# Performance work log

Measured on AMD Instinct MI355X. Metric: run time of the kernel, lower is better.

The kernel has to match this reference:

```python
import jax, jax.numpy as jnp
import numpy as np

B, CTX, DRAFT, D = 2, 4096, 512, 2048
H, KVH, HD = 16, 4, 128
N_REP = H // KVH
EPS = 1e-6
THETA = 10000.0
SCALE = 1.0 / np.sqrt(HD).astype(np.float32)


def setup_inputs() -> dict:
    key = jax.random.key(0)
    ks = jax.random.split(key, 6)
    return {
        "draft_hidden": jax.random.normal(ks[0], (B, DRAFT, D), jnp.float32),
        "context_hidden": jax.random.normal(ks[1], (B, CTX, D), jnp.float32),
        "Wq": jax.random.normal(ks[2], (H * HD, D), jnp.float32) * 0.02,
        "Wk": jax.random.normal(ks[3], (KVH * HD, D), jnp.float32) * 0.02,
        "Wv": jax.random.normal(ks[4], (KVH * HD, D), jnp.float32) * 0.02,
        "Wo": jax.random.normal(ks[5], (D, H * HD), jnp.float32) * 0.02,
        "q_norm_w": jnp.ones((HD,), jnp.float32),
        "k_norm_w": jnp.ones((HD,), jnp.float32),
        "context_position_ids": jnp.broadcast_to(jnp.arange(CTX, dtype=jnp.int32), (B, CTX)),
        "draft_position_ids": jnp.broadcast_to(CTX + jnp.arange(DRAFT, dtype=jnp.int32), (B, DRAFT)),
    }


def _rms_norm(x, w):
    # per-head RMSNorm over last dim (head_dim), computed in fp32
    v = jnp.mean(jnp.square(x.astype(jnp.float32)), axis=-1, keepdims=True)
    return (w * (x.astype(jnp.float32) * jax.lax.rsqrt(v + EPS))).astype(x.dtype)


def _rotate_half(x):
    x1, x2 = jnp.split(x, 2, axis=-1)
    return jnp.concatenate((-x2, x1), axis=-1)


def _rope(x, pos):
    # x: [B, nH, S, HD], pos: [B, S] int -> cos/sin gathered per position
    inv_freq = 1.0 / (THETA ** (jnp.arange(0, HD, 2, dtype=jnp.float32) / HD))  # [HD/2]
    freqs = pos.astype(jnp.float32)[:, None, :, None] * inv_freq  # [B,1,S,HD/2]
    emb = jnp.concatenate((freqs, freqs), axis=-1)  # [B,1,S,HD]
    return x * jnp.cos(emb) + _rotate_half(x) * jnp.sin(emb)


def reference(draft_hidden, context_hidden, Wq, Wk, Wv, Wo, q_norm_w, k_norm_w,
              context_position_ids, draft_position_ids):
    bsz, draft_len, _ = draft_hidden.shape
    ctx_len = context_hidden.shape[1]
    total_len = ctx_len + draft_len

    # Q from draft hidden only
    q = (draft_hidden @ Wq.T).reshape(bsz, draft_len, H, HD)
    q = _rms_norm(q, q_norm_w).transpose(0, 2, 1, 3)  # [B,H,Sq,HD]

    # Dual-source KV: context then draft, shared projections
    kv_in = jnp.concatenate([context_hidden, draft_hidden], axis=1)  # [B,total,D]
    k = (kv_in @ Wk.T).reshape(bsz, total_len, KVH, HD)
    v = (kv_in @ Wv.T).reshape(bsz, total_len, KVH, HD).transpose(0, 2, 1, 3)
    k = _rms_norm(k, k_norm_w).transpose(0, 2, 1, 3)  # [B,KVH,total,HD]

    full_position_ids = jnp.concatenate([context_position_ids, draft_position_ids], axis=1)
    q = _rope(q, draft_position_ids)
    k = _rope(k, full_position_ids)

    # GQA expansion (repeat each kv head n_rep times contiguously)
    k = jnp.repeat(k, N_REP, axis=1)  # [B,H,total,HD]
    v = jnp.repeat(v, N_REP, axis=1)

    # full (unmasked) scaled dot-product attention, block_mask=None path
    scores = jnp.einsum('bhqd,bhkd->bhqk', q, k) * SCALE
    probs = jax.nn.softmax(scores, axis=-1)
    attn = jnp.einsum('bhqk,bhkd->bhqd', probs, v)  # [B,H,Sq,HD]

    attn = attn.transpose(0, 2, 1, 3).reshape(bsz, draft_len, H * HD)
    return attn @ Wo.T
```

## Files before the change

### kernel.cpp

```cpp
#include <hip/hip_runtime.h>
#include <stdint.h>

#define B_ 2
#define CTX_ 4096
#define DRAFT_ 512
#define D_ 2048
#define H_ 16
#define KVH_ 4
#define HD_ 128
#define TOT_ 4608
#define NSPLIT 4
#define SPLIT_LEN (TOT_ / NSPLIT)

using bf16x8 = __attribute__((ext_vector_type(8))) short;
using f32x4  = __attribute__((ext_vector_type(4))) float;

__device__ __forceinline__ unsigned short f2bf(float x) {
  unsigned int u = __float_as_uint(x);
  u += 0x7fffu + ((u >> 16) & 1u);
  return (unsigned short)(u >> 16);
}

__device__ __forceinline__ unsigned cvtpk(float lo, float hi) {
  unsigned r;
  asm("v_cvt_pk_bf16_f32 %0, %1, %2" : "=v"(r) : "v"(lo), "v"(hi));
  return r;
}

__device__ __forceinline__ void gload16(const void* g, void* l) {
  __builtin_amdgcn_global_load_lds((const __attribute__((address_space(1))) void*)g,
                                   (__attribute__((address_space(3))) void*)l, 16, 0, 0);
}

__global__ __launch_bounds__(256, 4)
void conv_kernel(const float* __restrict__ ctx, const float* __restrict__ draft,
                 const float* __restrict__ wq, const float* __restrict__ wk,
                 const float* __restrict__ wv, const float* __restrict__ wo,
                 unsigned short* __restrict__ kv, unsigned short* __restrict__ wqb,
                 unsigned short* __restrict__ wkb, unsigned short* __restrict__ wvb,
                 unsigned short* __restrict__ wob) {
  long t = (long)blockIdx.x * 256 + threadIdx.x;
  const long NKV = (long)B_ * TOT_ * D_ / 8;
  const long NWQ = 2048L * 2048 / 8;
  const long NWK = 512L * 2048 / 8;
  const float* src;
  unsigned short* dst;
  if (t < NKV) {
    long i = t * 8;
    int b = (int)(i / ((long)TOT_ * D_));
    long rem = i - (long)b * TOT_ * D_;
    int r = (int)(rem / D_);
    int c = (int)(rem - (long)r * D_);
    if (r < CTX_) src = ctx + ((long)(b * CTX_ + r)) * D_ + c;
    else          src = draft + ((long)(b * DRAFT_ + (r - CTX_))) * D_ + c;
    dst = kv + i;
  } else if (t < NKV + NWQ) {
    long l = t - NKV; src = wq + l * 8; dst = wqb + l * 8;
  } else if (t < NKV + NWQ + NWK) {
    long l = t - NKV - NWQ; src = wk + l * 8; dst = wkb + l * 8;
  } else if (t < NKV + NWQ + 2 * NWK) {
    long l = t - NKV - NWQ - NWK; src = wv + l * 8; dst = wvb + l * 8;
  } else {
    long l = t - NKV - NWQ - 2 * NWK; src = wo + l * 8; dst = wob + l * 8;
  }
  float4 a = ((const float4*)src)[0];
  float4 b4 = ((const float4*)src)[1];
  uint4 o;
  o.x = (unsigned)f2bf(a.x) | ((unsigned)f2bf(a.y) << 16);
  o.y = (unsigned)f2bf(a.z) | ((unsigned)f2bf(a.w) << 16);
  o.z = (unsigned)f2bf(b4.x) | ((unsigned)f2bf(b4.y) << 16);
  o.w = (unsigned)f2bf(b4.z) | ((unsigned)f2bf(b4.w) << 16);
  *((uint4*)dst) = o;
}

template <int BM, int BN>
__device__ __forceinline__ void gemm_body(const unsigned short* __restrict__ A,
                                          const unsigned short* __restrict__ W,
                                          float* __restrict__ C, int ld, int kLen,
                                          int N, unsigned short* lds) {
  constexpr int MT = BM / 32;
  constexpr int NT = BN / 32;
  constexpr int BUF = (BM + BN) * 64;
  const int tid = threadIdx.x;
  const int lane = tid & 63, wid = tid >> 6;
  const int g = lane >> 4, r16 = lane & 15;
  const int wm = wid >> 1, wn = wid & 1;

  f32x4 zero = {0.f, 0.f, 0.f, 0.f};
  f32x4 acc[MT][NT];
#pragma unroll
  for (int i = 0; i < MT; ++i)
#pragma unroll
    for (int j = 0; j < NT; ++j) acc[i][j] = zero;

  auto stage = [&](int kb, unsigned short* buf) {
    unsigned short* As = buf;
    unsigned short* Bs = buf + BM * 64;
#pragma unroll
    for (int is = 0; is < BM / 32; ++is) {
      int row = is * 32 + (tid >> 3);
      int sl = (tid & 7) ^ (row & 7);
      gload16(A + (long)row * ld + kb + sl * 8, As + is * 2048 + wid * 512);
    }
#pragma unroll
    for (int is = 0; is < BN / 32; ++is) {
      int row = is * 32 + (tid >> 3);
      int sl = (tid & 7) ^ (row & 7);
      gload16(W + (long)row * ld + kb + sl * 8, Bs + is * 2048 + wid * 512);
    }
  };

  stage(0, lds);
  const int nk = kLen >> 6;
  for (int t = 0; t < nk; ++t) {
    __syncthreads();
    if (t + 1 < nk) stage((t + 1) << 6, lds + ((t + 1) & 1) * BUF);
    unsigned short* As = lds + (t & 1) * BUF;
    unsigned short* Bs = As + BM * 64;
#pragma unroll
    for (int kh = 0; kh < 2; ++kh) {
      bf16x8 af[MT], bfr[NT];
#pragma unroll
      for (int i = 0; i < MT; ++i) {
        int row = wm * (BM / 2) + i * 16 + r16;
        int sl = (kh * 4 + g) ^ (row & 7);
        af[i] = *(const bf16x8*)(As + row * 64 + sl * 8);
      }
#pragma unroll
      for (int j = 0; j < NT; ++j) {
        int row = wn * (BN / 2) + j * 16 + r16;
        int sl = (kh * 4 + g) ^ (row & 7);
        bfr[j] = *(const bf16x8*)(Bs + row * 64 + sl * 8);
      }
#pragma unroll
      for (int i = 0; i < MT; ++i)
#pragma unroll
        for (int j = 0; j < NT; ++j)
          acc[i][j] = __builtin_amdgcn_mfma_f32_16x16x32_bf16(af[i], bfr[j], acc[i][j], 0, 0, 0);
    }
  }
#pragma unroll
  for (int i = 0; i < MT; ++i)
#pragma unroll
    for (int j = 0; j < NT; ++j)
#pragma unroll
      for (int e = 0; e < 4; ++e) {
        int row = wm * (BM / 2) + i * 16 + g * 4 + e;
        int col = wn * (BN / 2) + j * 16 + r16;
        C[(long)row * N + col] = acc[i][j][e];
      }
}

__global__ __launch_bounds__(256, 2)
void qkv_kernel(const unsigned short* __restrict__ kvb,
                const unsigned short* __restrict__ wqb,
                const unsigned short* __restrict__ wkvb, float* __restrict__ qraw,
                float* __restrict__ kvraw) {
  __shared__ unsigned short lds[2 * 256 * 64];
  int id = blockIdx.x;
  if (id < 128) {
    int b = id >> 6, mb = (id >> 4) & 3, nb = id & 15;
    const unsigned short* A = kvb + ((long)b * TOT_ + CTX_ + mb * 128) * 2048;
    const unsigned short* W = wqb + (long)nb * 128 * 2048;
    float* C = qraw + ((long)b * 512 + mb * 128) * 2048 + nb * 128;
    gemm_body<128, 128>(A, W, C, 2048, 2048, 2048, lds);
  } else {
    int id2 = id - 128;
    int mb = id2 >> 3, nb = id2 & 7;
    const unsigned short* A = kvb + (long)mb * 128 * 2048;
    const unsigned short* W = wkvb + (long)nb * 128 * 2048;
    float* C = kvraw + (long)mb * 128 * 1024 + nb * 128;
    gemm_body<128, 128>(A, W, C, 2048, 2048, 1024, lds);
  }
}

__global__ __launch_bounds__(256, 3)
void ogemm_kernel(const unsigned short* __restrict__ attb,
                  const unsigned short* __restrict__ wob, float* __restrict__ oP) {
  __shared__ unsigned short lds[2 * 192 * 64];
  int mb = blockIdx.x, nb = blockIdx.y, z = blockIdx.z;
  const unsigned short* A = attb + (long)mb * 64 * 2048 + z * 1024;
  const unsigned short* W = wob + (long)nb * 128 * 2048 + z * 1024;
  float* C = oP + (long)z * 1024 * 2048 + (long)mb * 64 * 2048 + nb * 128;
  gemm_body<64, 128>(A, W, C, 2048, 1024, 2048, lds);
}

__global__ __launch_bounds__(256, 4)
void addo_kernel(const float* __restrict__ oP, float* __restrict__ out) {
  long t = (long)blockIdx.x * 256 + threadIdx.x;
  float4 a = ((const float4*)oP)[t];
  float4 b = ((const float4*)(oP + 1024L * 2048))[t];
  ((float4*)out)[t] = make_float4(a.x + b.x, a.y + b.y, a.z + b.z, a.w + b.w);
}

__global__ __launch_bounds__(256, 4)
void post_kernel(const float* __restrict__ qraw, const float* __restrict__ kvraw,
                 const float* __restrict__ qw, const float* __restrict__ kw,
                 const int* __restrict__ cpos, const int* __restrict__ dpos,
                 unsigned short* __restrict__ qatt, unsigned short* __restrict__ katt,
                 unsigned short* __restrict__ vt) {
  const int QB = (B_ * DRAFT_ * H_) / 4;
  const int KB = (B_ * TOT_ * KVH_) / 4;
  int bid = blockIdx.x;
  int tid = threadIdx.x;
  int lane = tid & 63, wid = tid >> 6;
  if (bid < QB + KB) {
    bool isQ = (bid < QB);
    int row = (isQ ? bid : bid - QB) * 4 + wid;
    const float* src;
    const float* wnorm;
    int pos;
    float fold;
    unsigned short* dst;
    if (isQ) {
      int b = row >> 13;
      int r2 = row & 8191;
      int s = r2 >> 4, hh = r2 & 15;
      src = qraw + (long)row * 128;
      wnorm = qw;
      pos = dpos[b * DRAFT_ + s];
      fold = 0.08838834764831843f * 1.4426950408889634f;
      dst = qatt + ((long)(b * H_ + hh) * DRAFT_ + s) * 128;
    } else {
      int b = row / (TOT_ * KVH_);
      int r2 = row - b * (TOT_ * KVH_);
      int s = r2 >> 2, hh = r2 & 3;
      src = kvraw + ((long)(b * TOT_ + s)) * 1024 + hh * 128;
      wnorm = kw;
      pos = (s < CTX_) ? cpos[b * CTX_ + s] : dpos[b * DRAFT_ + (s - CTX_)];
      fold = 1.0f;
      dst = katt + ((long)(b * KVH_ + hh) * TOT_ + s) * 128;
    }
    float x1 = src[lane], x2 = src[lane + 64];
    float ss = x1 * x1 + x2 * x2;
#pragma unroll
    for (int off = 1; off < 64; off <<= 1) ss += __shfl_xor(ss, off);
    float rn = rsqrtf(ss * 0.0078125f + 1e-6f);
    float y1 = wnorm[lane] * x1 * rn;
    float y2 = wnorm[lane + 64] * x2 * rn;
    float invf = exp2f((float)lane * -0.20762050593046014f);
    float fr = (float)pos * invf;
    float sn, cs;
    sincosf(fr, &sn, &cs);
    dst[lane] = f2bf((y1 * cs - y2 * sn) * fold);
    dst[lane + 64] = f2bf((y2 * cs + y1 * sn) * fold);
  } else {
    long t = (long)(bid - (QB + KB)) * 256 + tid;
    int d = (int)(t & 127);
    int rest = (int)(t >> 7);
    int sc = rest % 576, bk = rest / 576;
    int b = bk >> 2, kvh = bk & 3;
    int s0 = sc * 8;
    const float* src = kvraw + ((long)(b * TOT_ + s0)) * 1024 + 512 + kvh * 128 + d;
    unsigned int o[4];
#pragma unroll
    for (int jj = 0; jj < 4; ++jj) {
      unsigned short lo = f2bf(src[(2 * jj) * 1024]);
      unsigned short hi = f2bf(src[(2 * jj + 1) * 1024]);
      o[jj] = (unsigned)lo | ((unsigned)hi << 16);
    }
    uint4 ov = make_uint4(o[0], o[1], o[2], o[3]);
    *((uint4*)(vt + ((long)(bk * 128 + d)) * TOT_ + s0)) = ov;
  }
}

__global__ __launch_bounds__(256, 2)
void attn_kernel(const unsigned short* __restrict__ Q, const unsigned short* __restrict__ Kt,
                 const unsigned short* __restrict__ Vt, float* __restrict__ pO,
                 float* __restrict__ pL) {
  __shared__ unsigned short lds[2 * 16384 + 8192];
  unsigned short* P = lds + 32768;
  const int tid = threadIdx.x, lane = tid & 63, wid = tid >> 6;
  const int g = lane >> 4, r16 = lane & 15;
  const int q0 = blockIdx.x, h = blockIdx.y;
  const int b = blockIdx.z >> 2, split = blockIdx.z & 3;
  const int kvh = h >> 2;
  const float M = 16.4f;

  const unsigned short* Qbase =
      Q + ((long)(b * H_ + h) * DRAFT_ + q0 * 128 + wid * 32) * 128;
  bf16x8 qf[2][4];
#pragma unroll
  for (int f = 0; f < 2; ++f)
#pragma unroll
    for (int kb = 0; kb < 4; ++kb)
      qf[f][kb] = *(const bf16x8*)(Qbase + (f * 16 + r16) * 128 + kb * 32 + g * 8);

  f32x4 acc[2][8];
#pragma unroll
  for (int f = 0; f < 2; ++f)
#pragma unroll
    for (int nb = 0; nb < 8; ++nb) acc[f][nb] = f32x4{0.f, 0.f, 0.f, 0.f};
  float l_run[2] = {0.f, 0.f};

  const unsigned short* Kbase = Kt + (long)(b * KVH_ + kvh) * TOT_ * 128;
  const unsigned short* Vbase = Vt + (long)(b * KVH_ + kvh) * 128L * TOT_;

  auto stage = [&](int s0, int c) {
    unsigned short* Ks = lds + c * 16384;
    unsigned short* Vs = Ks + 8192;
#pragma unroll
    for (int is = 0; is < 4; ++is) {
      int row = is * 16 + (tid >> 4);
      int sl = (tid & 15) ^ (row & 7);
      gload16(Kbase + (long)(s0 + row) * 128 + sl * 8, Ks + is * 2048 + wid * 512);
    }
#pragma unroll
    for (int is = 0; is < 4; ++is) {
      int d = is * 32 + (tid >> 3);
      int sl = (tid & 7) ^ (d & 7);
      gload16(Vbase + (long)d * TOT_ + s0 + sl * 8, Vs + is * 2048 + wid * 512);
    }
  };

  const int sBeg = split * SPLIT_LEN;
  const int NTile = SPLIT_LEN / 64;
  stage(sBeg, 0);
  int cur = 0;
  for (int t = 0; t < NTile; ++t) {
    if (t + 1 < NTile) {
      stage(sBeg + (t + 1) * 64, cur ^ 1);
      asm volatile("s_waitcnt vmcnt(8)" ::: "memory");
    } else {
      asm volatile("s_waitcnt vmcnt(0)" ::: "memory");
    }
    __builtin_amdgcn_s_barrier();
    __builtin_amdgcn_sched_barrier(0);
    const unsigned short* Ks = lds + cur * 16384;
    const unsigned short* Vs = Ks + 8192;

    f32x4 st[2][4];
#pragma unroll
    for (int f = 0; f < 2; ++f)
#pragma unroll
      for (int h2 = 0; h2 < 4; ++h2) st[f][h2] = f32x4{-M, -M, -M, -M};
    __builtin_amdgcn_s_setprio(1);
#pragma unroll
    for (int h2 = 0; h2 < 4; ++h2) {
      int row = h2 * 16 + r16;
#pragma unroll
      for (int kb = 0; kb < 4; ++kb) {
        int sl = (kb * 4 + g) ^ (row & 7);
        bf16x8 a = *(const bf16x8*)(Ks + row * 128 + sl * 8);
        st[0][h2] = __builtin_amdgcn_mfma_f32_16x16x32_bf16(a, qf[0][kb], st[0][h2], 0, 0, 0);
        st[1][h2] = __builtin_amdgcn_mfma_f32_16x16x32_bf16(a, qf[1][kb], st[1][h2], 0, 0, 0);
      }
    }
    __builtin_amdgcn_s_setprio(0);

#pragma unroll
    for (int f = 0; f < 2; ++f) {
      float tsum = 0.0f;
#pragma unroll
      for (int h2 = 0; h2 < 4; ++h2)
#pragma unroll
        for (int e = 0; e < 4; ++e) {
          float p = exp2f(st[f][h2][e]);
          st[f][h2][e] = p;
          tsum += p;
        }
      tsum += __shfl_xor(tsum, 16);
      tsum += __shfl_xor(tsum, 32);
      l_run[f] += tsum;
      int qr = wid * 32 + f * 16 + r16;
#pragma unroll
      for (int h2 = 0; h2 < 4; ++h2) {
        unsigned lo = cvtpk(st[f][h2][0], st[f][h2][1]);
        unsigned hi = cvtpk(st[f][h2][2], st[f][h2][3]);
        int gr = (h2 * 2 + (g >> 1)) ^ (qr & 7);
        *(uint2*)((char*)P + qr * 128 + gr * 16 + (g & 1) * 8) = make_uint2(lo, hi);
      }
    }
    bf16x8 pb[2][2];
#pragma unroll
    for (int f = 0; f < 2; ++f) {
      int qr = wid * 32 + f * 16 + r16;
#pragma unroll
      for (int kb2 = 0; kb2 < 2; ++kb2) {
        int gr = (kb2 * 4 + g) ^ (qr & 7);
        pb[f][kb2] = *(const bf16x8*)((const char*)P + qr * 128 + gr * 16);
      }
    }
    __builtin_amdgcn_s_setprio(1);
#pragma unroll
    for (int nb = 0; nb < 8; ++nb) {
      int d = nb * 16 + r16;
#pragma unroll
      for (int kb2 = 0; kb2 < 2; ++kb2) {
        int sl = (kb2 * 4 + g) ^ (d & 7);
        bf16x8 a = *(const bf16x8*)(Vs + d * 64 + sl * 8);
        acc[0][nb] = __builtin_amdgcn_mfma_f32_16x16x32_bf16(a, pb[0][kb2], acc[0][nb], 0, 0, 0);
        acc[1][nb] = __builtin_amdgcn_mfma_f32_16x16x32_bf16(a, pb[1][kb2], acc[1][nb], 0, 0, 0);
      }
    }
    __builtin_amdgcn_s_setprio(0);
    __builtin_amdgcn_sched_barrier(0);
    __builtin_amdgcn_s_barrier();
    cur ^= 1;
  }

  const long R = (long)B_ * H_ * DRAFT_;
#pragma unroll
  for (int f = 0; f < 2; ++f) {
    int q = q0 * 128 + wid * 32 + f * 16 + r16;
    long rowIdx = ((long)(b * H_ + h)) * DRAFT_ + q;
    long pbase = ((long)split * R + rowIdx) * 128;
#pragma unroll
    for (int nb = 0; nb < 8; ++nb)
#pragma unroll
      for (int e = 0; e < 4; ++e) pO[pbase + nb * 16 + g * 4 + e] = acc[f][nb][e];
    if (g == 0) pL[(long)split * R + rowIdx] = l_run[f];
  }
}

__global__ __launch_bounds__(256, 4)
void acomb_kernel(const float* __restrict__ pO, const float* __restrict__ pL,
                  unsigned short* __restrict__ attb) {
  const long R = (long)B_ * H_ * DRAFT_;
  int row = blockIdx.x * 2 + (threadIdx.x >> 7);
  int d = threadIdx.x & 127;
  float ltot = 0.0f, o = 0.0f;
#pragma unroll
  for (int i = 0; i < NSPLIT; ++i) {
    ltot += pL[(long)i * R + row];
    o += pO[((long)i * R + row) * 128 + d];
  }
  o /= ltot;
  int bh = row >> 9, q = row & 511;
  int b = bh >> 4, h = bh & 15;
  attb[(((long)(b * 512 + q) * 16 + h)) * 128 + d] = f2bf(o);
}

extern "C" void kernel_launch(void* const* d_in, const int* in_sizes, int n_in,
                              void* d_out, int out_size, void* d_ws, size_t ws_size,
                              hipStream_t stream) {
  const float* draft = (const float*)d_in[0];
  const float* ctx = (const float*)d_in[1];
  const float* Wq = (const float*)d_in[2];
  const float* Wk = (const float*)d_in[3];
  const float* Wv = (const float*)d_in[4];
  const float* Wo = (const float*)d_in[5];
  const float* qw = (const float*)d_in[6];
  const float* kw = (const float*)d_in[7];
  const int* cpos = (const int*)d_in[8];
  const int* dpos = (const int*)d_in[9];

  char* ws = (char*)d_ws;
  unsigned short* kvb = (unsigned short*)(ws + 0);
  float* oP = (float*)(ws + 0);
  unsigned short* wqb = (unsigned short*)(ws + 37748736);
  unsigned short* wkb = (unsigned short*)(ws + 46137344);
  unsigned short* wvb = (unsigned short*)(ws + 48234496);
  unsigned short* wob = (unsigned short*)(ws + 50331648);
  float* qraw = (float*)(ws + 58720256);
  float* kvraw = (float*)(ws + 67108864);
  float* pO = (float*)(ws + 67108864);
  float* pL = (float*)(ws + 100663296);
  unsigned short* qatt = (unsigned short*)(ws + 104857600);
  unsigned short* katt = (unsigned short*)(ws + 109051904);
  unsigned short* vtb = (unsigned short*)(ws + 118489088);
  unsigned short* attb = (unsigned short*)(ws + 127926272);

  conv_kernel<<<dim3(14336), 256, 0, stream>>>(ctx, draft, Wq, Wk, Wv, Wo, kvb, wqb,
                                               wkb, wvb, wob);
  qkv_kernel<<<dim3(704), 256, 0, stream>>>(kvb, wqb, wkb, qraw, kvraw);
  post_kernel<<<dim3(15616), 256, 0, stream>>>(qraw, kvraw, qw, kw, cpos, dpos, qatt,
                                               katt, vtb);
  attn_kernel<<<dim3(4, 16, 2 * NSPLIT), 256, 0, stream>>>(qatt, katt, vtb, pO, pL);
  acomb_kernel<<<dim3(8192), 256, 0, stream>>>(pO, pL, attb);
  ogemm_kernel<<<dim3(16, 16, 2), 256, 0, stream>>>(attb, wob, oP);
  addo_kernel<<<dim3(2048), 256, 0, stream>>>(oP, (float*)d_out);
}
```

Measured before the change: 193.8 us.

## Switch attention to 32x32x16 MFMA with register-resident P and permuted V layout

Rewrites the attention inner loop to use 32x32x16 bf16 MFMAs, so the exponentiated score fragments can be repacked in registers as the B operand of the PV product. This drops the P round trip through LDS. The post kernel now writes V-transpose with a permuted k-order so it matches the 32x32 accumulator layout, and output stores become float4. Blocks of the attention and QKV GEMM grids are also remapped in an XCD-aware order to improve L2 locality. The main risks are register pressure from the larger accumulators and silent wrong results if the V permutation and the fragment mapping do not match exactly.

Result: faster. 180.9 us (-6.7%).

```diff
diff --git a/kernel.cpp b/kernel.cpp
--- a/kernel.cpp
+++ b/kernel.cpp
@@ -14,6 +14,7 @@
 
 using bf16x8 = __attribute__((ext_vector_type(8))) short;
 using f32x4  = __attribute__((ext_vector_type(4))) float;
+using f32x16 = __attribute__((ext_vector_type(16))) float;
 
 __device__ __forceinline__ unsigned short f2bf(float x) {
   unsigned int u = __float_as_uint(x);
@@ -30,6 +31,13 @@
 __device__ __forceinline__ void gload16(const void* g, void* l) {
   __builtin_amdgcn_global_load_lds((const __attribute__((address_space(1))) void*)g,
                                    (__attribute__((address_space(3))) void*)l, 16, 0, 0);
+}
+
+__device__ __forceinline__ f32x16 vbroad16(float x) {
+  f32x16 v;
+#pragma unroll
+  for (int i = 0; i < 16; ++i) v[i] = x;
+  return v;
 }
 
 __global__ __launch_bounds__(256, 4)
@@ -157,7 +165,7 @@
                 const unsigned short* __restrict__ wkvb, float* __restrict__ qraw,
                 float* __restrict__ kvraw) {
   __shared__ unsigned short lds[2 * 256 * 64];
-  int id = blockIdx.x;
+  int id = (blockIdx.x & 7) * 88 + (blockIdx.x >> 3);
   if (id < 128) {
     int b = id >> 6, mb = (id >> 4) & 3, nb = id & 15;
     const unsigned short* A = kvb + ((long)b * TOT_ + CTX_ + mb * 128) * 2048;
@@ -259,8 +267,10 @@
       unsigned short hi = f2bf(src[(2 * jj + 1) * 1024]);
       o[jj] = (unsigned)lo | ((unsigned)hi << 16);
     }
-    uint4 ov = make_uint4(o[0], o[1], o[2], o[3]);
-    *((uint4*)(vt + ((long)(bk * 128 + d)) * TOT_ + s0)) = ov;
+    int k0 = s0 & 63;
+    long dstbase = ((long)(bk * 128 + d)) * TOT_ + (s0 & ~63) + (k0 & 48) + ((k0 & 8) >> 1);
+    *(uint2*)(vt + dstbase) = make_uint2(o[0], o[1]);
+    *(uint2*)(vt + dstbase + 8) = make_uint2(o[2], o[3]);
   }
 }
 
@@ -268,30 +278,26 @@
 void attn_kernel(const unsigned short* __restrict__ Q, const unsigned short* __restrict__ Kt,
                  const unsigned short* __restrict__ Vt, float* __restrict__ pO,
                  float* __restrict__ pL) {
-  __shared__ unsigned short lds[2 * 16384 + 8192];
-  unsigned short* P = lds + 32768;
+  __shared__ unsigned short lds[2 * 16384];
   const int tid = threadIdx.x, lane = tid & 63, wid = tid >> 6;
-  const int g = lane >> 4, r16 = lane & 15;
-  const int q0 = blockIdx.x, h = blockIdx.y;
-  const int b = blockIdx.z >> 2, split = blockIdx.z & 3;
+  const int hi = lane >> 5, l31 = lane & 31;
+  int sw = ((blockIdx.x & 7) << 6) | (blockIdx.x >> 3);
+  const int q0 = sw & 3, h = (sw >> 2) & 15, z = sw >> 6;
+  const int b = z >> 2, split = z & 3;
   const int kvh = h >> 2;
   const float M = 16.4f;
 
-  const unsigned short* Qbase =
+  const unsigned short* Qb =
       Q + ((long)(b * H_ + h) * DRAFT_ + q0 * 128 + wid * 32) * 128;
-  bf16x8 qf[2][4];
-#pragma unroll
-  for (int f = 0; f < 2; ++f)
-#pragma unroll
-    for (int kb = 0; kb < 4; ++kb)
-      qf[f][kb] = *(const bf16x8*)(Qbase + (f * 16 + r16) * 128 + kb * 32 + g * 8);
-
-  f32x4 acc[2][8];
-#pragma unroll
-  for (int f = 0; f < 2; ++f)
-#pragma unroll
-    for (int nb = 0; nb < 8; ++nb) acc[f][nb] = f32x4{0.f, 0.f, 0.f, 0.f};
-  float l_run[2] = {0.f, 0.f};
+  bf16x8 qf[8];
+#pragma unroll
+  for (int ks = 0; ks < 8; ++ks)
+    qf[ks] = *(const bf16x8*)(Qb + l31 * 128 + ks * 16 + hi * 8);
+
+  f32x16 acc[4];
+#pragma unroll
+  for (int nb = 0; nb < 4; ++nb) acc[nb] = vbroad16(0.f);
+  float l_run = 0.0f;
 
   const unsigned short* Kbase = Kt + (long)(b * KVH_ + kvh) * TOT_ * 128;
   const unsigned short* Vbase = Vt + (long)(b * KVH_ + kvh) * 128L * TOT_;
@@ -326,71 +332,53 @@
     }
     __builtin_amdgcn_s_barrier();
     __builtin_amdgcn_sched_barrier(0);
-    const unsigned short* Ks = lds + cur * 16384;
-    const unsigned short* Vs = Ks + 8192;
-
-    f32x4 st[2][4];
-#pragma unroll
-    for (int f = 0; f < 2; ++f)
-#pragma unroll
-      for (int h2 = 0; h2 < 4; ++h2) st[f][h2] = f32x4{-M, -M, -M, -M};
+    const char* KsB = (const char*)(lds + cur * 16384);
+    const char* VsB = KsB + 16384;
+
+    f32x16 st0 = vbroad16(-M), st1 = vbroad16(-M);
     __builtin_amdgcn_s_setprio(1);
 #pragma unroll
-    for (int h2 = 0; h2 < 4; ++h2) {
-      int row = h2 * 16 + r16;
-#pragma unroll
-      for (int kb = 0; kb < 4; ++kb) {
-        int sl = (kb * 4 + g) ^ (row & 7);
-        bf16x8 a = *(const bf16x8*)(Ks + row * 128 + sl * 8);
-        st[0][h2] = __builtin_amdgcn_mfma_f32_16x16x32_bf16(a, qf[0][kb], st[0][h2], 0, 0, 0);
-        st[1][h2] = __builtin_amdgcn_mfma_f32_16x16x32_bf16(a, qf[1][kb], st[1][h2], 0, 0, 0);
-      }
+    for (int ks = 0; ks < 8; ++ks) {
+      int gsl = ks * 2 + hi;
+      bf16x8 a0 = *(const bf16x8*)(KsB + l31 * 256 + ((gsl ^ (l31 & 7)) * 16));
+      bf16x8 a1 = *(const bf16x8*)(KsB + (32 + l31) * 256 + ((gsl ^ (l31 & 7)) * 16));
+      st0 = __builtin_amdgcn_mfma_f32_32x32x16_bf16(a0, qf[ks], st0, 0, 0, 0);
+      st1 = __builtin_amdgcn_mfma_f32_32x32x16_bf16(a1, qf[ks], st1, 0, 0, 0);
     }
     __builtin_amdgcn_s_setprio(0);
 
-#pragma unroll
-    for (int f = 0; f < 2; ++f) {
-      float tsum = 0.0f;
-#pragma unroll
-      for (int h2 = 0; h2 < 4; ++h2)
-#pragma unroll
-        for (int e = 0; e < 4; ++e) {
-          float p = exp2f(st[f][h2][e]);
-          st[f][h2][e] = p;
-          tsum += p;
-        }
-      tsum += __shfl_xor(tsum, 16);
-      tsum += __shfl_xor(tsum, 32);
-      l_run[f] += tsum;
-      int qr = wid * 32 + f * 16 + r16;
-#pragma unroll
-      for (int h2 = 0; h2 < 4; ++h2) {
-        unsigned lo = cvtpk(st[f][h2][0], st[f][h2][1]);
-        unsigned hi = cvtpk(st[f][h2][2], st[f][h2][3]);
-        int gr = (h2 * 2 + (g >> 1)) ^ (qr & 7);
-        *(uint2*)((char*)P + qr * 128 + gr * 16 + (g & 1) * 8) = make_uint2(lo, hi);
-      }
-    }
-    bf16x8 pb[2][2];
-#pragma unroll
-    for (int f = 0; f < 2; ++f) {
-      int qr = wid * 32 + f * 16 + r16;
-#pragma unroll
-      for (int kb2 = 0; kb2 < 2; ++kb2) {
-        int gr = (kb2 * 4 + g) ^ (qr & 7);
-        pb[f][kb2] = *(const bf16x8*)((const char*)P + qr * 128 + gr * 16);
-      }
+    float l_own = 0.0f;
+    unsigned pkA[8], pkB[8];
+#pragma unroll
+    for (int m = 0; m < 8; ++m) {
+      float e0 = exp2f(st0[2 * m]), e1 = exp2f(st0[2 * m + 1]);
+      l_own += e0 + e1;
+      pkA[m] = cvtpk(e0, e1);
+    }
+#pragma unroll
+    for (int m = 0; m < 8; ++m) {
+      float e0 = exp2f(st1[2 * m]), e1 = exp2f(st1[2 * m + 1]);
+      l_own += e0 + e1;
+      pkB[m] = cvtpk(e0, e1);
+    }
+    l_run += l_own;
+
+    union { unsigned u[4]; bf16x8 v; } pf[4];
+#pragma unroll
+    for (int m = 0; m < 4; ++m) {
+      pf[0].u[m] = pkA[m];
+      pf[1].u[m] = pkA[m + 4];
+      pf[2].u[m] = pkB[m];
+      pf[3].u[m] = pkB[m + 4];
     }
     __builtin_amdgcn_s_setprio(1);
 #pragma unroll
-    for (int nb = 0; nb < 8; ++nb) {
-      int d = nb * 16 + r16;
-#pragma unroll
-      for (int kb2 = 0; kb2 < 2; ++kb2) {
-        int sl = (kb2 * 4 + g) ^ (d & 7);
-        bf16x8 a = *(const bf16x8*)(Vs + d * 64 + sl * 8);
-        acc[0][nb] = __builtin_amdgcn_mfma_f32_16x16x32_bf16(a, pb[0][kb2], acc[0][nb], 0, 0, 0);
-        acc[1][nb] = __builtin_amdgcn_mfma_f32_16x16x32_bf16(a, pb[1][kb2], acc[1][nb], 0, 0, 0);
+    for (int nb = 0; nb < 4; ++nb) {
+      int d = nb * 32 + l31;
+#pragma unroll
+      for (int ks2 = 0; ks2 < 4; ++ks2) {
+        bf16x8 a = *(const bf16x8*)(VsB + d * 128 + (((ks2 * 2 + hi) ^ (d & 7)) * 16));
+        acc[nb] = __builtin_amdgcn_mfma_f32_32x32x16_bf16(a, pf[ks2].v, acc[nb], 0, 0, 0);
       }
     }
     __builtin_amdgcn_s_setprio(0);
@@ -398,19 +386,22 @@
     __builtin_amdgcn_s_barrier();
     cur ^= 1;
   }
+  l_run += __shfl_xor(l_run, 32);
 
   const long R = (long)B_ * H_ * DRAFT_;
-#pragma unroll
-  for (int f = 0; f < 2; ++f) {
-    int q = q0 * 128 + wid * 32 + f * 16 + r16;
-    long rowIdx = ((long)(b * H_ + h)) * DRAFT_ + q;
-    long pbase = ((long)split * R + rowIdx) * 128;
-#pragma unroll
-    for (int nb = 0; nb < 8; ++nb)
-#pragma unroll
-      for (int e = 0; e < 4; ++e) pO[pbase + nb * 16 + g * 4 + e] = acc[f][nb][e];
-    if (g == 0) pL[(long)split * R + rowIdx] = l_run[f];
-  }
+  const int q = q0 * 128 + wid * 32 + l31;
+  const long rowIdx = ((long)(b * H_ + h)) * DRAFT_ + q;
+  const long pbase = ((long)split * R + rowIdx) * 128;
+#pragma unroll
+  for (int nb = 0; nb < 4; ++nb)
+#pragma unroll
+    for (int r4 = 0; r4 < 4; ++r4) {
+      int d0 = nb * 32 + 8 * r4 + 4 * hi;
+      float4 v = make_float4(acc[nb][4 * r4 + 0], acc[nb][4 * r4 + 1],
+                             acc[nb][4 * r4 + 2], acc[nb][4 * r4 + 3]);
+      *(float4*)(pO + pbase + d0) = v;
+    }
+  if (hi == 0) pL[(long)split * R + rowIdx] = l_run;
 }
 
 __global__ __launch_bounds__(256, 4)
@@ -466,7 +457,7 @@
   qkv_kernel<<<dim3(704), 256, 0, stream>>>(kvb, wqb, wkb, qraw, kvraw);
   post_kernel<<<dim3(15616), 256, 0, stream>>>(qraw, kvraw, qw, kw, cpos, dpos, qatt,
                                                katt, vtb);
-  attn_kernel<<<dim3(4, 16, 2 * NSPLIT), 256, 0, stream>>>(qatt, katt, vtb, pO, pL);
+  attn_kernel<<<dim3(512), 256, 0, stream>>>(qatt, katt, vtb, pO, pL);
   acomb_kernel<<<dim3(8192), 256, 0, stream>>>(pO, pL, attb);
   ogemm_kernel<<<dim3(16, 16, 2), 256, 0, stream>>>(attb, wob, oP);
   addo_kernel<<<dim3(2048), 256, 0, stream>>>(oP, (float*)d_out);
```
